# Kernel tuning notes

Hardware: AMD Instinct MI355X
Metric: run time of the kernel (lower is better)

The kernel has to match this reference:

```python
import jax, jax.numpy as jnp
import numpy as np

N_WORDS, L, VOCAB, D = 8192, 24, 128, 512
H, DK = 8, 64  # n_head, d_v (=d_k)
N_NAMES, WORDS_PER_NAME = 2048, 4
N_CONCEPTS, NAMES_PER_CONCEPT = 256, 8


def setup_inputs() -> dict:
    key = jax.random.key(0)
    ks = jax.random.split(key, 9)
    s = 1.0 / np.sqrt(D).astype(np.float32)
    inputs = jax.random.randint(ks[0], (N_WORDS, L), 0, VOCAB)  # 0 = pad char
    n_words = jnp.full((N_NAMES,), WORDS_PER_NAME, dtype=jnp.int32)
    n_names = jnp.full((N_CONCEPTS,), NAMES_PER_CONCEPT, dtype=jnp.int32)
    return {
        "inputs": inputs,
        "n_words": n_words,
        "n_names": n_names,
        "emb": jax.random.normal(ks[1], (VOCAB, D), jnp.float32) * s,
        "Wq": jax.random.normal(ks[2], (D, H * DK), jnp.float32) * s,
        "Wk": jax.random.normal(ks[3], (D, H * DK), jnp.float32) * s,
        "Wv": jax.random.normal(ks[4], (D, H * DK), jnp.float32) * s,
        "Wo": jax.random.normal(ks[5], (H * DK, D), jnp.float32) * s,
        "W1": jax.random.normal(ks[6], (D, 512), jnp.float32) * s,
        "W2": jax.random.normal(ks[7], (512, 256), jnp.float32) * s,
    }


def reference(inputs, n_words, n_names, emb, Wq, Wk, Wv, Wo, W1, W2):
    N, Lq = inputs.shape
    pad = inputs == 0  # [N, L] padding mask (char id 0)

    # --- MHAEncoder: embedding + masked multi-head self-attention ---
    x = emb[inputs]  # [N, L, D]
    def split_heads(t):  # [N, L, H*DK] -> [N, H, L, DK]
        return t.reshape(N, Lq, H, DK).transpose(0, 2, 1, 3)
    q = split_heads(x @ Wq)
    k = split_heads(x @ Wk)
    v = split_heads(x @ Wv)
    scale = jnp.asarray(1.0 / np.sqrt(DK), x.dtype)
    scores = jnp.einsum('nhqd,nhkd->nhqk', q, k) * scale  # [N, H, L, L]
    scores = jnp.where(pad[:, None, None, :], jnp.asarray(-1e9, x.dtype), scores)
    attn = jax.nn.softmax(scores, axis=-1)
    o = jnp.einsum('nhqk,nhkd->nhqd', attn, v)
    word_ft = o.transpose(0, 2, 1, 3).reshape(N, Lq, H * DK) @ Wo  # [N, L, D]

    # --- masked mean pooling over chars: matmul(mask, word_ft)/mask.sum(-1) ---
    m = (~pad).astype(word_ft.dtype)  # [N, L]
    name_emb = jnp.einsum('nl,nld->nd', m, word_ft) / m.sum(-1, keepdims=True)  # [N, D]

    # --- split(n_words) + per-group mean == segment mean over word groups ---
    G = n_words.shape[0]
    seg = jnp.repeat(jnp.arange(G), n_words, total_repeat_length=N)
    name_ft = jax.ops.segment_sum(name_emb, seg, num_segments=G)
    name_ft = name_ft / n_words[:, None].astype(name_ft.dtype)  # [G, D]

    # --- small no-bias Tanh MLP ---
    h = jnp.tanh(name_ft @ W1)
    out = jnp.tanh(h @ W2)  # [G, 256]
    # final .split(n_names) is a view-only regrouping; return the packed array
    return out
```

## Files before the change

kernel.cpp:

```cpp
#include <hip/hip_runtime.h>
#include <math.h>

#define NWORDS 8192
#define LW     24
#define VOC    128
#define DIM    512
#define NH     8
#define DKH    64
#define GNAMES 2048
#define F2     256

#define S1_LEN 458752

#define GEMM_BODY(A_, B_, K_, N_, m0_, n0_, kbeg_, kchunk_)                         \
  __shared__ float As[2][16][68];                                                   \
  __shared__ float Bs[2][16][68];                                                   \
  const int t = threadIdx.x, tx = t & 15, ty = t >> 4;                              \
  float acc[4][4] = {};                                                             \
  float ra[4], rb[4];                                                               \
  _Pragma("unroll")                                                                 \
  for (int i = 0; i < 4; ++i) { int idx = t + 256 * i;                              \
    ra[i] = A_[(size_t)(m0_ + (idx >> 4)) * K_ + kbeg_ + (idx & 15)]; }             \
  _Pragma("unroll")                                                                 \
  for (int i = 0; i < 4; ++i) { int idx = t + 256 * i;                              \
    rb[i] = B_[(size_t)(kbeg_ + (idx >> 6)) * N_ + n0_ + (idx & 63)]; }             \
  _Pragma("unroll")                                                                 \
  for (int i = 0; i < 4; ++i) { int idx = t + 256 * i; As[0][idx & 15][idx >> 4] = ra[i]; } \
  _Pragma("unroll")                                                                 \
  for (int i = 0; i < 4; ++i) { int idx = t + 256 * i; Bs[0][idx >> 6][idx & 63] = rb[i]; } \
  __syncthreads();                                                                  \
  int buf = 0;                                                                      \
  for (int k0 = kbeg_; k0 < kbeg_ + kchunk_; k0 += 16) {                            \
    const bool more = (k0 + 16 < kbeg_ + kchunk_);                                  \
    if (more) {                                                                     \
      _Pragma("unroll")                                                             \
      for (int i = 0; i < 4; ++i) { int idx = t + 256 * i;                          \
        ra[i] = A_[(size_t)(m0_ + (idx >> 4)) * K_ + (k0 + 16) + (idx & 15)]; }     \
      _Pragma("unroll")                                                             \
      for (int i = 0; i < 4; ++i) { int idx = t + 256 * i;                          \
        rb[i] = B_[(size_t)(k0 + 16 + (idx >> 6)) * N_ + n0_ + (idx & 63)]; }       \
    }                                                                               \
    _Pragma("unroll")                                                               \
    for (int k = 0; k < 16; ++k) {                                                  \
      float a[4], b[4];                                                             \
      _Pragma("unroll")                                                             \
      for (int i = 0; i < 4; ++i) a[i] = As[buf][k][ty * 4 + i];                    \
      _Pragma("unroll")                                                             \
      for (int j = 0; j < 4; ++j) b[j] = Bs[buf][k][tx * 4 + j];                    \
      _Pragma("unroll")                                                             \
      for (int i = 0; i < 4; ++i)                                                   \
        _Pragma("unroll")                                                           \
        for (int j = 0; j < 4; ++j) acc[i][j] += a[i] * b[j];                       \
    }                                                                               \
    if (more) {                                                                     \
      _Pragma("unroll")                                                             \
      for (int i = 0; i < 4; ++i) { int idx = t + 256 * i; As[buf ^ 1][idx & 15][idx >> 4] = ra[i]; } \
      _Pragma("unroll")                                                             \
      for (int i = 0; i < 4; ++i) { int idx = t + 256 * i; Bs[buf ^ 1][idx >> 6][idx & 63] = rb[i]; } \
      __syncthreads();                                                              \
      buf ^= 1;                                                                     \
    }                                                                               \
  }

template<int NSPLIT>
__global__ __launch_bounds__(256) void k_stage1(const float* __restrict__ emb,
                                                const float* __restrict__ Wq,
                                                const float* __restrict__ Wk,
                                                const float* __restrict__ Wv,
                                                const float* __restrict__ Wo,
                                                const float* __restrict__ W1,
                                                float* __restrict__ P) {
  const int tid = blockIdx.x, s = blockIdx.y;
  const float *A, *B;
  int coff, m0, n0;
  if (tid < 48) {
    const int g = tid >> 4, mt = tid & 15;
    A = emb;
    B = (g == 0) ? Wq : ((g == 1) ? Wk : Wv);
    coff = g * 65536;
    m0 = (mt >> 3) * 64; n0 = (mt & 7) * 64;
  } else {
    const int id = tid - 48;
    A = Wo; B = W1; coff = 3 * 65536;
    m0 = (id >> 3) * 64; n0 = (id & 7) * 64;
  }
  const int kchunk = 512 / NSPLIT, kbeg = s * kchunk;
  GEMM_BODY(A, B, 512, 512, m0, n0, kbeg, kchunk)
  float* Cp = P + (size_t)s * S1_LEN + coff;
  #pragma unroll
  for (int i = 0; i < 4; ++i) {
    float4 v = make_float4(acc[i][0], acc[i][1], acc[i][2], acc[i][3]);
    *(float4*)&Cp[(size_t)(m0 + ty * 4 + i) * 512 + n0 + tx * 4] = v;
  }
}

template<int ACT>
__global__ __launch_bounds__(256) void k_gemm64(const float* __restrict__ A,
                                                const float* __restrict__ B,
                                                float* __restrict__ C,
                                                int M, int N, int K, int kchunk) {
  const int m0 = blockIdx.y * 64, n0 = blockIdx.x * 64;
  const int kbeg = blockIdx.z * kchunk;
  GEMM_BODY(A, B, K, N, m0, n0, kbeg, kchunk)
  float* Cp = C + (size_t)blockIdx.z * M * N;
  #pragma unroll
  for (int i = 0; i < 4; ++i) {
    float4 v = make_float4(acc[i][0], acc[i][1], acc[i][2], acc[i][3]);
    if (ACT) { v.x = tanhf(v.x); v.y = tanhf(v.y); v.z = tanhf(v.z); v.w = tanhf(v.w); }
    *(float4*)&Cp[(size_t)(m0 + ty * 4 + i) * N + n0 + tx * 4] = v;
  }
}

template<int ACT, int S>
__global__ __launch_bounds__(256) void k_reduce(const float* __restrict__ P,
                                                float* __restrict__ O,
                                                int len4, int stride4) {
  const int i = blockIdx.x * 256 + threadIdx.x;
  if (i >= len4) return;
  const float4* P4 = (const float4*)P;
  float4 a = P4[i];
  #pragma unroll
  for (int s = 1; s < S; ++s) {
    float4 b = P4[(size_t)s * stride4 + i];
    a.x += b.x; a.y += b.y; a.z += b.z; a.w += b.w;
  }
  if (ACT) { a.x = tanhf(a.x); a.y = tanhf(a.y); a.z = tanhf(a.z); a.w = tanhf(a.w); }
  ((float4*)O)[i] = a;
}

__global__ __launch_bounds__(128) void k_qk_tab(const float* __restrict__ EQ,
                                                const float* __restrict__ EK,
                                                float* __restrict__ etab) {
  const int c1 = blockIdx.x, h = blockIdx.y, c2 = threadIdx.x;
  __shared__ float qrow[DKH];
  if (threadIdx.x < DKH) qrow[threadIdx.x] = EQ[c1 * DIM + h * DKH + threadIdx.x];
  __syncthreads();
  const float* krow = EK + c2 * DIM + h * DKH;
  float acc = 0.f;
  #pragma unroll
  for (int d = 0; d < DKH; ++d) acc += qrow[d] * krow[d];
  etab[((size_t)c1 * VOC + c2) * NH + h] = __expf(acc * 0.125f);
}

__global__ __launch_bounds__(256) void k_scan(const int* __restrict__ nw, int* __restrict__ offs) {
  __shared__ int part[256];
  const int t = threadIdx.x;
  int v[8]; int s = 0;
  #pragma unroll
  for (int i = 0; i < 8; ++i) { v[i] = nw[t * 8 + i]; s += v[i]; }
  part[t] = s;
  __syncthreads();
  if (t == 0) {
    int a = 0;
    for (int i = 0; i < 256; ++i) { int x = part[i]; part[i] = a; a += x; }
    offs[GNAMES] = a;
  }
  __syncthreads();
  int a = part[t];
  #pragma unroll
  for (int i = 0; i < 8; ++i) { offs[t * 8 + i] = a; a += v[i]; }
}

__global__ __launch_bounds__(192) void k_attn(const int* __restrict__ inputs,
                                              const int* __restrict__ offs,
                                              const float* __restrict__ etab,
                                              const float* __restrict__ EV,
                                              float* __restrict__ NP) {
  const int g = blockIdx.x, t = threadIdx.x;
  const int o0 = offs[g], o1 = offs[g + 1];
  __shared__ int   cs[LW];
  __shared__ float wpart[3][NH][25];
  const int q = t >> 3, h = t & 7;
  const int wv = t >> 6, lane = t & 63;
  float4 acc = make_float4(0.f, 0.f, 0.f, 0.f);

  for (int wi = o0; wi < o1; ++wi) {
    __syncthreads();
    if (t < LW) cs[t] = inputs[(size_t)wi * LW + t];
    __syncthreads();

    const int cq = cs[q];
    float row[LW];
    float inv = 0.f;
    if (cq != 0) {
      const float* tb = etab + (size_t)cq * (VOC * NH) + h;
      float sum = 0.f;
      #pragma unroll
      for (int kp = 0; kp < LW; ++kp) {
        int ck = cs[kp];
        float e = (ck != 0) ? tb[(size_t)ck * NH] : 0.f;
        row[kp] = e; sum += e;
      }
      inv = 1.f / sum;
    } else {
      #pragma unroll
      for (int kp = 0; kp < LW; ++kp) row[kp] = 0.f;
    }
    #pragma unroll
    for (int kp = 0; kp < LW; ++kp) {
      float v = row[kp] * inv;
      v += __shfl_xor(v, 8, 64);
      v += __shfl_xor(v, 16, 64);
      v += __shfl_xor(v, 32, 64);
      if (lane < 8) wpart[wv][lane][kp] = v;
    }
    int cnt = 0;
    #pragma unroll
    for (int l = 0; l < LW; ++l) cnt += (cs[l] != 0);
    __syncthreads();

    if (t < 128) {
      const float invc = cnt ? 1.f / (float)cnt : 0.f;
      const int hh = t >> 4;
      const float4* EV4 = (const float4*)EV;
      float4 a2 = make_float4(0.f, 0.f, 0.f, 0.f);
      #pragma unroll
      for (int kp = 0; kp < LW; ++kp) {
        int ck = cs[kp];
        if (ck != 0) {
          float w = wpart[0][hh][kp] + wpart[1][hh][kp] + wpart[2][hh][kp];
          float4 ev = EV4[(size_t)ck * (DIM / 4) + t];
          a2.x += w * ev.x; a2.y += w * ev.y; a2.z += w * ev.z; a2.w += w * ev.w;
        }
      }
      acc.x += invc * a2.x; acc.y += invc * a2.y;
      acc.z += invc * a2.z; acc.w += invc * a2.w;
    }
  }
  if (t < 128) {
    const float invn = (o1 > o0) ? 1.f / (float)(o1 - o0) : 0.f;
    acc.x *= invn; acc.y *= invn; acc.z *= invn; acc.w *= invn;
    ((float4*)NP)[(size_t)g * (DIM / 4) + t] = acc;
  }
}

extern "C" void kernel_launch(void* const* d_in, const int* in_sizes, int n_in,
                              void* d_out, int out_size, void* d_ws, size_t ws_size,
                              hipStream_t stream) {
  const int*   inputs  = (const int*)d_in[0];
  const int*   n_words = (const int*)d_in[1];
  const float* emb     = (const float*)d_in[3];
  const float* Wq      = (const float*)d_in[4];
  const float* Wk      = (const float*)d_in[5];
  const float* Wv      = (const float*)d_in[6];
  const float* Wo      = (const float*)d_in[7];
  const float* W1      = (const float*)d_in[8];
  const float* W2      = (const float*)d_in[9];
  float* out = (float*)d_out;

  float* ws  = (float*)d_ws;
  float* ES  = ws;
  float* BIG = ws + 458752;
  float* TAB = ws + 1507328;
  float* NP  = ws + 1638400;
  float* H1  = ws + 2686976;
  int*  OFFS = (int*)(ws + 3735552);

  k_scan<<<1, 256, 0, stream>>>(n_words, OFFS);
  k_stage1<2><<<dim3(112, 2), 256, 0, stream>>>(emb, Wq, Wk, Wv, Wo, W1, BIG);
  k_reduce<0, 2><<<S1_LEN / 4 / 256, 256, 0, stream>>>(BIG, ES, S1_LEN / 4, S1_LEN / 4);
  k_qk_tab<<<dim3(VOC, NH), 128, 0, stream>>>(ES, ES + 65536, TAB);
  k_attn<<<GNAMES, 192, 0, stream>>>(inputs, OFFS, TAB, ES + 131072, NP);
  k_gemm64<1><<<dim3(8, 32, 1), 256, 0, stream>>>(NP, ES + 196608, H1, 2048, 512, 512, 512);
  k_gemm64<0><<<dim3(4, 32, 2), 256, 0, stream>>>(H1, W2, BIG, 2048, F2, 512, 256);
  k_reduce<1, 2><<<(GNAMES * F2) / 4 / 256, 256, 0, stream>>>(BIG, out, (GNAMES * F2) / 4, (GNAMES * F2) / 4);
}
```

Before: 121.4 us.

## Restructure attention kernel to per-wave words and add split-K to GEMMs

The attention kernel now gives each wavefront its own word, using ballot/shuffle for the char codes and counts. It also drops the per-word block barriers and the shared-memory weight reduction, reducing across waves once at the end. The qk table zeroes pad entries so lookups need no branch. Stage1 and both MLP GEMMs use more split-K partitions with separate reduce kernels to raise parallelism. This costs extra workspace traffic and one extra kernel launch.

```diff
diff --git a/kernel.cpp b/kernel.cpp
--- a/kernel.cpp
+++ b/kernel.cpp
@@ -139,7 +139,8 @@
   float acc = 0.f;
   #pragma unroll
   for (int d = 0; d < DKH; ++d) acc += qrow[d] * krow[d];
-  etab[((size_t)c1 * VOC + c2) * NH + h] = __expf(acc * 0.125f);
+  float e = (c1 != 0 && c2 != 0) ? __expf(acc * 0.125f) : 0.f;
+  etab[((size_t)c1 * VOC + c2) * NH + h] = e;
 }
 
 __global__ __launch_bounds__(256) void k_scan(const int* __restrict__ nw, int* __restrict__ offs) {
@@ -161,77 +162,76 @@
   for (int i = 0; i < 8; ++i) { offs[t * 8 + i] = a; a += v[i]; }
 }
 
-__global__ __launch_bounds__(192) void k_attn(const int* __restrict__ inputs,
-                                              const int* __restrict__ offs,
-                                              const float* __restrict__ etab,
-                                              const float* __restrict__ EV,
-                                              float* __restrict__ NP) {
+__global__ __launch_bounds__(256, 8) void k_attn(const int* __restrict__ inputs,
+                                                 const int* __restrict__ offs,
+                                                 const float* __restrict__ etab,
+                                                 const float* __restrict__ EV,
+                                                 float* __restrict__ NP) {
   const int g = blockIdx.x, t = threadIdx.x;
+  const int wv = t >> 6, l = t & 63;
+  const int h = l & 7, qg = l >> 3;
+  const int tl = qg | (h << 3);
   const int o0 = offs[g], o1 = offs[g + 1];
-  __shared__ int   cs[LW];
-  __shared__ float wpart[3][NH][25];
-  const int q = t >> 3, h = t & 7;
-  const int wv = t >> 6, lane = t & 63;
-  float4 acc = make_float4(0.f, 0.f, 0.f, 0.f);
-
-  for (int wi = o0; wi < o1; ++wi) {
-    __syncthreads();
-    if (t < LW) cs[t] = inputs[(size_t)wi * LW + t];
-    __syncthreads();
-
-    const int cq = cs[q];
-    float row[LW];
-    float inv = 0.f;
-    if (cq != 0) {
-      const float* tb = etab + (size_t)cq * (VOC * NH) + h;
-      float sum = 0.f;
-      #pragma unroll
-      for (int kp = 0; kp < LW; ++kp) {
-        int ck = cs[kp];
-        float e = (ck != 0) ? tb[(size_t)ck * NH] : 0.f;
-        row[kp] = e; sum += e;
-      }
-      inv = 1.f / sum;
-    } else {
-      #pragma unroll
-      for (int kp = 0; kp < LW; ++kp) row[kp] = 0.f;
-    }
+  __shared__ float red[4][DIM];
+
+  float4 accA = make_float4(0.f, 0.f, 0.f, 0.f);
+  float4 accB = make_float4(0.f, 0.f, 0.f, 0.f);
+
+  for (int wi = o0 + wv; wi < o1; wi += 4) {
+    int c_l = (l < LW) ? inputs[(size_t)wi * LW + l] : 0;
+    unsigned long long mk = __ballot(c_l != 0);
+    int cnt = __popcll(mk);
+    float invc = cnt ? 1.f / (float)cnt : 0.f;
+
+    int cq0 = __shfl(c_l, qg);
+    int cq1 = __shfl(c_l, qg + 8);
+    int cq2 = __shfl(c_l, qg + 16);
+    const float* b0 = etab + (cq0 << 10) + h;
+    const float* b1 = etab + (cq1 << 10) + h;
+    const float* b2 = etab + (cq2 << 10) + h;
+
+    float d0 = 0.f, d1 = 0.f, d2 = 0.f;
     #pragma unroll
     for (int kp = 0; kp < LW; ++kp) {
-      float v = row[kp] * inv;
-      v += __shfl_xor(v, 8, 64);
-      v += __shfl_xor(v, 16, 64);
-      v += __shfl_xor(v, 32, 64);
-      if (lane < 8) wpart[wv][lane][kp] = v;
+      int o = __shfl(c_l, kp) << 3;
+      d0 += b0[o]; d1 += b1[o]; d2 += b2[o];
     }
-    int cnt = 0;
+    float i0 = cq0 ? invc / d0 : 0.f;
+    float i1 = cq1 ? invc / d1 : 0.f;
+    float i2 = cq2 ? invc / d2 : 0.f;
+
     #pragma unroll
-    for (int l = 0; l < LW; ++l) cnt += (cs[l] != 0);
-    __syncthreads();
-
-    if (t < 128) {
-      const float invc = cnt ? 1.f / (float)cnt : 0.f;
-      const int hh = t >> 4;
-      const float4* EV4 = (const float4*)EV;
-      float4 a2 = make_float4(0.f, 0.f, 0.f, 0.f);
-      #pragma unroll
-      for (int kp = 0; kp < LW; ++kp) {
-        int ck = cs[kp];
-        if (ck != 0) {
-          float w = wpart[0][hh][kp] + wpart[1][hh][kp] + wpart[2][hh][kp];
-          float4 ev = EV4[(size_t)ck * (DIM / 4) + t];
-          a2.x += w * ev.x; a2.y += w * ev.y; a2.z += w * ev.z; a2.w += w * ev.w;
-        }
+    for (int kp = 0; kp < LW; ++kp) {
+      int ck = __shfl(c_l, kp);
+      if (ck) {
+        int o = ck << 3;
+        float v = b0[o] * i0 + b1[o] * i1 + b2[o] * i2;
+        v += __shfl_xor(v, 8);
+        v += __shfl_xor(v, 16);
+        v += __shfl_xor(v, 32);
+        float w = __shfl(v, tl);
+        const float4* evr = (const float4*)EV + (ck << 7) + (l << 1);
+        float4 ea = evr[0], eb = evr[1];
+        accA.x += w * ea.x; accA.y += w * ea.y; accA.z += w * ea.z; accA.w += w * ea.w;
+        accB.x += w * eb.x; accB.y += w * eb.y; accB.z += w * eb.z; accB.w += w * eb.w;
       }
-      acc.x += invc * a2.x; acc.y += invc * a2.y;
-      acc.z += invc * a2.z; acc.w += invc * a2.w;
     }
   }
-  if (t < 128) {
-    const float invn = (o1 > o0) ? 1.f / (float)(o1 - o0) : 0.f;
-    acc.x *= invn; acc.y *= invn; acc.z *= invn; acc.w *= invn;
-    ((float4*)NP)[(size_t)g * (DIM / 4) + t] = acc;
-  }
+
+  ((float4*)&red[wv][l * 8])[0] = accA;
+  ((float4*)&red[wv][l * 8])[1] = accB;
+  __syncthreads();
+
+  const float invn = (o1 > o0) ? 1.f / (float)(o1 - o0) : 0.f;
+  const int j = t * 2;
+  float2 s0 = *(const float2*)&red[0][j];
+  float2 s1 = *(const float2*)&red[1][j];
+  float2 s2 = *(const float2*)&red[2][j];
+  float2 s3 = *(const float2*)&red[3][j];
+  float2 r;
+  r.x = (s0.x + s1.x + s2.x + s3.x) * invn;
+  r.y = (s0.y + s1.y + s2.y + s3.y) * invn;
+  *(float2*)&NP[(size_t)g * DIM + j] = r;
 }
 
 extern "C" void kernel_launch(void* const* d_in, const int* in_sizes, int n_in,
@@ -251,17 +251,18 @@
   float* ws  = (float*)d_ws;
   float* ES  = ws;
   float* BIG = ws + 458752;
-  float* TAB = ws + 1507328;
-  float* NP  = ws + 1638400;
-  float* H1  = ws + 2686976;
-  int*  OFFS = (int*)(ws + 3735552);
+  float* TAB = ws + 2555904;
+  float* NP  = ws + 2686976;
+  float* H1  = ws + 3735552;
+  int*  OFFS = (int*)(ws + 4784128);
 
   k_scan<<<1, 256, 0, stream>>>(n_words, OFFS);
-  k_stage1<2><<<dim3(112, 2), 256, 0, stream>>>(emb, Wq, Wk, Wv, Wo, W1, BIG);
-  k_reduce<0, 2><<<S1_LEN / 4 / 256, 256, 0, stream>>>(BIG, ES, S1_LEN / 4, S1_LEN / 4);
+  k_stage1<4><<<dim3(112, 4), 256, 0, stream>>>(emb, Wq, Wk, Wv, Wo, W1, BIG);
+  k_reduce<0, 4><<<S1_LEN / 4 / 256, 256, 0, stream>>>(BIG, ES, S1_LEN / 4, S1_LEN / 4);
   k_qk_tab<<<dim3(VOC, NH), 128, 0, stream>>>(ES, ES + 65536, TAB);
-  k_attn<<<GNAMES, 192, 0, stream>>>(inputs, OFFS, TAB, ES + 131072, NP);
-  k_gemm64<1><<<dim3(8, 32, 1), 256, 0, stream>>>(NP, ES + 196608, H1, 2048, 512, 512, 512);
-  k_gemm64<0><<<dim3(4, 32, 2), 256, 0, stream>>>(H1, W2, BIG, 2048, F2, 512, 256);
-  k_reduce<1, 2><<<(GNAMES * F2) / 4 / 256, 256, 0, stream>>>(BIG, out, (GNAMES * F2) / 4, (GNAMES * F2) / 4);
-}
+  k_attn<<<GNAMES, 256, 0, stream>>>(inputs, OFFS, TAB, ES + 131072, NP);
+  k_gemm64<0><<<dim3(8, 32, 2), 256, 0, stream>>>(NP, ES + 196608, BIG, 2048, 512, 512, 256);
+  k_reduce<1, 2><<<(GNAMES * DIM) / 4 / 256, 256, 0, stream>>>(BIG, H1, (GNAMES * DIM) / 4, (GNAMES * DIM) / 4);
+  k_gemm64<0><<<dim3(4, 32, 4), 256, 0, stream>>>(H1, W2, BIG, 2048, F2, 512, 128);
+  k_reduce<1, 4><<<(GNAMES * F2) / 4 / 256, 256, 0, stream>>>(BIG, out, (GNAMES * F2) / 4, (GNAMES * F2) / 4);
+}
```

New measurement: 136.7 us. 12.6% more time.
